# Kernel tuning notes

Hardware: AMD Instinct MI355X
Metric: run time of the kernel (lower is better)

The kernel has to match this reference:

```python
import jax, jax.numpy as jnp
import numpy as np

B = 8192
NUM_DRUGS = 4000
NUM_CELL_LINES = 64
D0 = 128
D1 = 128


def setup_inputs() -> dict:
    key = jax.random.key(0)
    k1, k2, k3, k4, k5 = jax.random.split(key, 5)
    drug_pairs = jax.random.randint(k1, (B, 2), 0, NUM_DRUGS, dtype=jnp.int64)
    cell_lines = jax.random.randint(k2, (B,), 0, NUM_CELL_LINES, dtype=jnp.int64)
    h_drug = jax.random.normal(k3, (NUM_DRUGS, D0), dtype=jnp.float32)
    predictor_lin = 0.01 * jax.random.normal(k4, (NUM_CELL_LINES, D0, D1), dtype=jnp.float32)
    predictor_prod = 0.01 * jax.random.normal(k5, (NUM_CELL_LINES, D1, D1), dtype=jnp.float32)
    return {"drug_pairs": drug_pairs, "cell_lines": cell_lines, "h_drug": h_drug,
            "predictor_lin": predictor_lin, "predictor_prod": predictor_prod}


def reference(drug_pairs, cell_lines, h_drug, predictor_lin, predictor_prod):
    # Gather per-sample cell-line-specific linear weights: [B, D0, D1]
    W = predictor_lin[cell_lines]
    h1 = h_drug[drug_pairs[:, 0]]  # [B, D0]
    h2 = h_drug[drug_pairs[:, 1]]  # [B, D0]
    h1 = jax.nn.relu(jnp.einsum('bd,bdh->bh', h1, W))  # [B, D1]
    h2 = jax.nn.relu(jnp.einsum('bd,bdh->bh', h2, W))  # [B, D1]
    # Symmetric bilinear form G = P + P^T, per sample
    P = predictor_prod[cell_lines]  # [B, D1, D1]
    G = P + jnp.swapaxes(P, 1, 2)
    # score = <h1, G h2>
    return jnp.einsum('bh,bhk,bk->b', h1, G, h2)
```

## Files before the change

### kernel.cpp

```cpp
#include <hip/hip_runtime.h>

#define D        128
#define CH       32
#define TPB      256
#define EPP      4
#define LIST_CAP 128

__global__ __launch_bounds__(TPB, 2) void ipp_main(
    const int* __restrict__ dp, const int* __restrict__ cl,
    const float* __restrict__ hd, const float* __restrict__ W_all,
    const float* __restrict__ P_all, float* __restrict__ out,
    int B, int range)
{
    __shared__ float  sx[8][D];
    __shared__ float  sh[8][D];
    __shared__ float4 part[4][8][32];
    __shared__ int    list[LIST_CAP];
    __shared__ int    lcount;

    const int tid   = threadIdx.x;
    const int c     = blockIdx.x / CH;
    const int chunk = blockIdx.x % CH;
    const int g     = tid >> 5;
    const int c4    = tid & 31;
    const int wv    = tid >> 6;

    if (tid == 0) lcount = 0;
    __syncthreads();

    {
        const int base = chunk * range;
        const int end  = min(base + range, B);
        for (int j = base + tid; j < end; j += TPB)
            if (cl[j] == c) {
                int p = atomicAdd(&lcount, 1);
                if (p < LIST_CAP) list[p] = j;
            }
    }

    float4 Wreg[16], Preg[16];
    {
        const float4* gW = (const float4*)(W_all + (size_t)c * D * D);
        const float4* gP = (const float4*)(P_all + (size_t)c * D * D);
        #pragma unroll
        for (int dd = 0; dd < 16; ++dd) {
            Wreg[dd] = gW[(g * 16 + dd) * 32 + c4];
            Preg[dd] = gP[(g * 16 + dd) * 32 + c4];
        }
    }
    __syncthreads();
    const int n = min(lcount, LIST_CAP);

#define FMA4(A_, S_, W_)                                                       \
    (A_).x = fmaf((S_), (W_).x, (A_).x);                                       \
    (A_).y = fmaf((S_), (W_).y, (A_).y);                                       \
    (A_).z = fmaf((S_), (W_).z, (A_).z);                                       \
    (A_).w = fmaf((S_), (W_).w, (A_).w);

#define MATTILE(SRC, REG)                                                      \
    {                                                                          \
        _Pragma("unroll")                                                      \
        for (int q = 0; q < 4; ++q) {                                          \
            _Pragma("unroll")                                                  \
            for (int r = 0; r < 8; ++r) {                                      \
                const float4 xq = ((const float4*)(SRC)[r])[g * 4 + q];        \
                float4& ac = acc[r >> 1][r & 1];                               \
                FMA4(ac, xq.x, REG[q * 4 + 0])                                 \
                FMA4(ac, xq.y, REG[q * 4 + 1])                                 \
                FMA4(ac, xq.z, REG[q * 4 + 2])                                 \
                FMA4(ac, xq.w, REG[q * 4 + 3])                                 \
            }                                                                  \
        }                                                                      \
        _Pragma("unroll")                                                      \
        for (int e = 0; e < EPP; ++e) {                                        \
            _Pragma("unroll")                                                  \
            for (int op = 0; op < 2; ++op) {                                   \
                float4& ac = acc[e][op];                                       \
                ac.x += __shfl_xor(ac.x, 32, 64);                              \
                ac.y += __shfl_xor(ac.y, 32, 64);                              \
                ac.z += __shfl_xor(ac.z, 32, 64);                              \
                ac.w += __shfl_xor(ac.w, 32, 64);                              \
            }                                                                  \
        }                                                                      \
        if ((tid & 32) == 0) {                                                 \
            _Pragma("unroll")                                                  \
            for (int r = 0; r < 8; ++r)                                        \
                part[wv][r][c4] = acc[r >> 1][r & 1];                          \
        }                                                                      \
    }

    const int npass = (n + EPP - 1) / EPP;
    for (int pass = 0; pass < npass; ++pass) {
        const int pbase = pass * EPP;

        {
            const int e  = g >> 1, op = g & 1;
            const int pe = pbase + e;
            const int b  = list[pe < n ? pe : 0];
            const int dr = dp[2 * b + op];
            ((float4*)sx[g])[c4] = ((const float4*)(hd + (size_t)dr * D))[c4];
        }
        __syncthreads();

        float4 acc[EPP][2];
        #pragma unroll
        for (int e = 0; e < EPP; ++e)
            #pragma unroll
            for (int op = 0; op < 2; ++op)
                acc[e][op] = make_float4(0.f, 0.f, 0.f, 0.f);
        MATTILE(sx, Wreg)
        __syncthreads();
        {
            const float4 s0 = part[0][g][c4], s1 = part[1][g][c4];
            const float4 s2 = part[2][g][c4], s3 = part[3][g][c4];
            float4 s;
            s.x = fmaxf(s0.x + s1.x + s2.x + s3.x, 0.f);
            s.y = fmaxf(s0.y + s1.y + s2.y + s3.y, 0.f);
            s.z = fmaxf(s0.z + s1.z + s2.z + s3.z, 0.f);
            s.w = fmaxf(s0.w + s1.w + s2.w + s3.w, 0.f);
            ((float4*)sh[g])[c4] = s;
        }
        __syncthreads();

        #pragma unroll
        for (int e = 0; e < EPP; ++e)
            #pragma unroll
            for (int op = 0; op < 2; ++op)
                acc[e][op] = make_float4(0.f, 0.f, 0.f, 0.f);
        MATTILE(sh, Preg)
        __syncthreads();
        {
            const float4 s0 = part[0][g][c4], s1 = part[1][g][c4];
            const float4 s2 = part[2][g][c4], s3 = part[3][g][c4];
            float4 s;
            s.x = s0.x + s1.x + s2.x + s3.x;
            s.y = s0.y + s1.y + s2.y + s3.y;
            s.z = s0.z + s1.z + s2.z + s3.z;
            s.w = s0.w + s1.w + s2.w + s3.w;
            ((float4*)sx[g])[c4] = s;
        }
        __syncthreads();

        {
            const int e  = tid >> 6;
            const int k2 = (tid & 63) * 2;
            const float* t1 = sx[2 * e],     * t2 = sx[2 * e + 1];
            const float* h1 = sh[2 * e],     * h2 = sh[2 * e + 1];
            float prt = t1[k2] * h2[k2] + t1[k2 + 1] * h2[k2 + 1]
                      + t2[k2] * h1[k2] + t2[k2 + 1] * h1[k2 + 1];
            #pragma unroll
            for (int off = 32; off; off >>= 1)
                prt += __shfl_down(prt, off, 64);
            const int pe = pbase + e;
            if ((tid & 63) == 0 && pe < n) out[list[pe]] = prt;
        }
        __syncthreads();
    }
#undef MATTILE
#undef FMA4
}

extern "C" void kernel_launch(void* const* d_in, const int* in_sizes, int n_in,
                              void* d_out, int out_size, void* d_ws, size_t ws_size,
                              hipStream_t stream) {
    const int*   dp    = (const int*)  d_in[0];
    const int*   cl    = (const int*)  d_in[1];
    const float* hd    = (const float*)d_in[2];
    const float* W_all = (const float*)d_in[3];
    const float* P_all = (const float*)d_in[4];
    float*       out   = (float*)d_out;

    const int B     = out_size;
    const int ncl   = in_sizes[4] / (D * D);
    const int range = (B + CH - 1) / CH;

    ipp_main<<<dim3(ncl * CH), dim3(TPB), 0, stream>>>(
        dp, cl, hd, W_all, P_all, out, B, range);
}
```

Measured before the change: 110.8 us.

## Use 512-thread blocks with two sub-groups and prefetch first drug rows

Each block now has two independent 256-thread sub-groups. Each sub-group works on its own set of four samples, using separate shared-memory buffers. Chunks per cell line are halved, so each block scans twice the index range. The first drug embedding gather is issued before the per-thread W/P register loads, so the two global-load latencies overlap. The cost is that the launch bounds now require more resident threads per CU. With 128 floats of weights held in registers per thread, that may cap VGPRs tightly enough to cause spills.

```diff
diff --git a/kernel.cpp b/kernel.cpp
--- a/kernel.cpp
+++ b/kernel.cpp
@@ -1,8 +1,8 @@
 #include <hip/hip_runtime.h>
 
 #define D        128
-#define CH       32
-#define TPB      256
+#define CH       16
+#define TPB      512
 #define EPP      4
 #define LIST_CAP 128
 
@@ -12,18 +12,20 @@
     const float* __restrict__ P_all, float* __restrict__ out,
     int B, int range)
 {
-    __shared__ float  sx[8][D];
-    __shared__ float  sh[8][D];
-    __shared__ float4 part[4][8][32];
+    __shared__ float  sx[2][8][D];
+    __shared__ float  sh[2][8][D];
+    __shared__ float4 part[2][4][8][32];
     __shared__ int    list[LIST_CAP];
     __shared__ int    lcount;
 
-    const int tid   = threadIdx.x;
-    const int c     = blockIdx.x / CH;
-    const int chunk = blockIdx.x % CH;
-    const int g     = tid >> 5;
-    const int c4    = tid & 31;
-    const int wv    = tid >> 6;
+    const int tid  = threadIdx.x;
+    const int c    = blockIdx.x / CH;
+    const int chunk= blockIdx.x % CH;
+    const int sub  = tid >> 8;
+    const int stid = tid & 255;
+    const int g    = stid >> 5;
+    const int c4   = stid & 31;
+    const int wv   = stid >> 6;
 
     if (tid == 0) lcount = 0;
     __syncthreads();
@@ -37,6 +39,17 @@
                 if (p < LIST_CAP) list[p] = j;
             }
     }
+    __syncthreads();
+    const int n     = min(lcount, LIST_CAP);
+    const int npass = (n + 2 * EPP - 1) / (2 * EPP);
+
+    float4 xv = make_float4(0.f, 0.f, 0.f, 0.f);
+    if (n > 0) {
+        const int pe = 0 * 2 * EPP + sub * EPP + (g >> 1);
+        const int b  = list[pe < n ? pe : 0];
+        const int dr = dp[2 * b + (g & 1)];
+        xv = ((const float4*)(hd + (size_t)dr * D))[c4];
+    }
 
     float4 Wreg[16], Preg[16];
     {
@@ -48,8 +61,6 @@
             Preg[dd] = gP[(g * 16 + dd) * 32 + c4];
         }
     }
-    __syncthreads();
-    const int n = min(lcount, LIST_CAP);
 
 #define FMA4(A_, S_, W_)                                                       \
     (A_).x = fmaf((S_), (W_).x, (A_).x);                                       \
@@ -57,7 +68,7 @@
     (A_).z = fmaf((S_), (W_).z, (A_).z);                                       \
     (A_).w = fmaf((S_), (W_).w, (A_).w);
 
-#define MATTILE(SRC, REG)                                                      \
+#define MATTILE(SRC, REG, OUT)                                                 \
     {                                                                          \
         _Pragma("unroll")                                                      \
         for (int q = 0; q < 4; ++q) {                                          \
@@ -82,24 +93,23 @@
                 ac.w += __shfl_xor(ac.w, 32, 64);                              \
             }                                                                  \
         }                                                                      \
-        if ((tid & 32) == 0) {                                                 \
+        if ((stid & 32) == 0) {                                                \
             _Pragma("unroll")                                                  \
             for (int r = 0; r < 8; ++r)                                        \
-                part[wv][r][c4] = acc[r >> 1][r & 1];                          \
+                (OUT)[wv][r][c4] = acc[r >> 1][r & 1];                         \
         }                                                                      \
     }
 
-    const int npass = (n + EPP - 1) / EPP;
     for (int pass = 0; pass < npass; ++pass) {
-        const int pbase = pass * EPP;
+        const int pbase = pass * 2 * EPP + sub * EPP;
 
-        {
-            const int e  = g >> 1, op = g & 1;
-            const int pe = pbase + e;
+        if (pass > 0) {
+            const int pe = pbase + (g >> 1);
             const int b  = list[pe < n ? pe : 0];
-            const int dr = dp[2 * b + op];
-            ((float4*)sx[g])[c4] = ((const float4*)(hd + (size_t)dr * D))[c4];
+            const int dr = dp[2 * b + (g & 1)];
+            xv = ((const float4*)(hd + (size_t)dr * D))[c4];
         }
+        ((float4*)sx[sub][g])[c4] = xv;
         __syncthreads();
 
         float4 acc[EPP][2];
@@ -108,17 +118,17 @@
             #pragma unroll
             for (int op = 0; op < 2; ++op)
                 acc[e][op] = make_float4(0.f, 0.f, 0.f, 0.f);
-        MATTILE(sx, Wreg)
+        MATTILE(sx[sub], Wreg, part[sub])
         __syncthreads();
         {
-            const float4 s0 = part[0][g][c4], s1 = part[1][g][c4];
-            const float4 s2 = part[2][g][c4], s3 = part[3][g][c4];
+            const float4 s0 = part[sub][0][g][c4], s1 = part[sub][1][g][c4];
+            const float4 s2 = part[sub][2][g][c4], s3 = part[sub][3][g][c4];
             float4 s;
             s.x = fmaxf(s0.x + s1.x + s2.x + s3.x, 0.f);
             s.y = fmaxf(s0.y + s1.y + s2.y + s3.y, 0.f);
             s.z = fmaxf(s0.z + s1.z + s2.z + s3.z, 0.f);
             s.w = fmaxf(s0.w + s1.w + s2.w + s3.w, 0.f);
-            ((float4*)sh[g])[c4] = s;
+            ((float4*)sh[sub][g])[c4] = s;
         }
         __syncthreads();
 
@@ -127,32 +137,32 @@
             #pragma unroll
             for (int op = 0; op < 2; ++op)
                 acc[e][op] = make_float4(0.f, 0.f, 0.f, 0.f);
-        MATTILE(sh, Preg)
+        MATTILE(sh[sub], Preg, part[sub])
         __syncthreads();
         {
-            const float4 s0 = part[0][g][c4], s1 = part[1][g][c4];
-            const float4 s2 = part[2][g][c4], s3 = part[3][g][c4];
+            const float4 s0 = part[sub][0][g][c4], s1 = part[sub][1][g][c4];
+            const float4 s2 = part[sub][2][g][c4], s3 = part[sub][3][g][c4];
             float4 s;
             s.x = s0.x + s1.x + s2.x + s3.x;
             s.y = s0.y + s1.y + s2.y + s3.y;
             s.z = s0.z + s1.z + s2.z + s3.z;
             s.w = s0.w + s1.w + s2.w + s3.w;
-            ((float4*)sx[g])[c4] = s;
+            ((float4*)sx[sub][g])[c4] = s;
         }
         __syncthreads();
 
         {
-            const int e  = tid >> 6;
-            const int k2 = (tid & 63) * 2;
-            const float* t1 = sx[2 * e],     * t2 = sx[2 * e + 1];
-            const float* h1 = sh[2 * e],     * h2 = sh[2 * e + 1];
+            const int e  = stid >> 6;
+            const int k2 = (stid & 63) * 2;
+            const float* t1 = sx[sub][2 * e], * t2 = sx[sub][2 * e + 1];
+            const float* h1 = sh[sub][2 * e], * h2 = sh[sub][2 * e + 1];
             float prt = t1[k2] * h2[k2] + t1[k2 + 1] * h2[k2 + 1]
                       + t2[k2] * h1[k2] + t2[k2 + 1] * h1[k2 + 1];
             #pragma unroll
             for (int off = 32; off; off >>= 1)
                 prt += __shfl_down(prt, off, 64);
             const int pe = pbase + e;
-            if ((tid & 63) == 0 && pe < n) out[list[pe]] = prt;
+            if ((stid & 63) == 0 && pe < n) out[list[pe]] = prt;
         }
         __syncthreads();
     }
```

Result: slower. 124.4 us (+12.3%).
